# Kernel tuning notes

Measured on AMD Instinct MI355X. Metric: run time of the kernel, lower is better.

Reference implementation:

```python
import jax, jax.numpy as jnp
import numpy as np

HID = 768; HEADS = 12; DH = 64; W = 256  # one-sided window (attention_window=512)
L = 2; VOCAB = 50265; FFN = 3072; NLAB = 8921; B = 2; S = 4096
NEG = -1e9


def _ln(x, s, b):
    m = x.mean(-1, keepdims=True)
    v = ((x - m) ** 2).mean(-1, keepdims=True)
    return (x - m) * jax.lax.rsqrt(v + 1e-5) * s + b


def setup_inputs() -> dict:
    key = jax.random.key(0)
    ks = iter(jax.random.split(key, 64))
    def n(shape, sd=0.02):
        return jax.random.normal(next(ks), shape, jnp.float32) * sd
    inp = {
        'input_ids': jax.random.randint(next(ks), (B, S), 0, VOCAB, dtype=jnp.int32),
        'attention_mask': jnp.ones((B, S), jnp.int32),
        'word_emb': n((VOCAB, HID)), 'pos_emb': n((S, HID)),
        'emb_ln_s': jnp.ones((HID,), jnp.float32), 'emb_ln_b': jnp.zeros((HID,), jnp.float32),
        'Wq': n((L, HID, HID)), 'bq': jnp.zeros((L, HID), jnp.float32),
        'Wk': n((L, HID, HID)), 'bk': jnp.zeros((L, HID), jnp.float32),
        'Wv': n((L, HID, HID)), 'bv': jnp.zeros((L, HID), jnp.float32),
        'Wqg': n((L, HID, HID)), 'bqg': jnp.zeros((L, HID), jnp.float32),
        'Wkg': n((L, HID, HID)), 'bkg': jnp.zeros((L, HID), jnp.float32),
        'Wvg': n((L, HID, HID)), 'bvg': jnp.zeros((L, HID), jnp.float32),
        'Wo': n((L, HID, HID)), 'bo': jnp.zeros((L, HID), jnp.float32),
        'ln1_s': jnp.ones((L, HID), jnp.float32), 'ln1_b': jnp.zeros((L, HID), jnp.float32),
        'W1': n((L, HID, FFN)), 'b1': jnp.zeros((L, FFN), jnp.float32),
        'W2': n((L, FFN, HID)), 'b2': jnp.zeros((L, HID), jnp.float32),
        'ln2_s': jnp.ones((L, HID), jnp.float32), 'ln2_b': jnp.zeros((L, HID), jnp.float32),
        'head_W': n((HID, NLAB)), 'head_b': jnp.zeros((NLAB,), jnp.float32),
    }
    return inp


def _forward(input_ids, attention_mask, word_emb, pos_emb, emb_ln_s, emb_ln_b,
             Wq, bq, Wk, bk, Wv, bv, Wqg, bqg, Wkg, bkg, Wvg, bvg, Wo, bo,
             ln1_s, ln1_b, W1, b1, W2, b2, ln2_s, ln2_b, head_W, head_b):
    Bc, Sc = input_ids.shape
    nc = Sc // W
    scale = 1.0 / np.sqrt(DH).astype(np.float32)
    # embeddings
    x = word_emb[input_ids] + pos_emb[None, :Sc]
    x = _ln(x, emb_ln_s, emb_ln_b)
    # static band masks: query pos c*W+p, key pos (c-1)*W+kk in the 3-chunk layout
    p = jnp.arange(W)
    kk = jnp.arange(3 * W)
    rel = kk[None, :] - W - p[:, None]                     # [W,3W] key_pos - query_pos
    cpos = (jnp.arange(nc)[:, None, None] - 1) * W + kk[None, None, :]  # [nc,1,3W]
    valid = (cpos >= 0) & (cpos < Sc) & (cpos != 0) & (jnp.abs(rel)[None, :, :] <= W)  # [nc,W,3W]
    am_keys = attention_mask[:, jnp.clip(cpos, 0, Sc - 1)] > 0  # [B,nc,1,3W]
    band_mask = valid[None] & am_keys                        # [B,nc,W,3W]

    def split_heads(t):
        return t.reshape(Bc, Sc, HEADS, DH).transpose(0, 2, 1, 3)

    def chunk3(t):  # [B,H,S,D] -> [B,H,nc,3W,D] keys/values of chunks c-1,c,c+1
        tp = jnp.pad(t, ((0, 0), (0, 0), (W, W), (0, 0)))
        tr = tp.reshape(Bc, HEADS, nc + 2, W, DH)
        return jnp.concatenate([tr[:, :, :-2], tr[:, :, 1:-1], tr[:, :, 2:]], axis=3)

    for l in range(L):
        q = split_heads(x @ Wq[l] + bq[l])
        k = split_heads(x @ Wk[l] + bk[l])
        v = split_heads(x @ Wv[l] + bv[l])
        qg = split_heads(x @ Wqg[l] + bqg[l])
        kg = split_heads(x @ Wkg[l] + bkg[l])
        vg = split_heads(x @ Wvg[l] + bvg[l])
        # sliding-window banded scores
        qc = q.reshape(Bc, HEADS, nc, W, DH)
        kc = chunk3(k)
        vc = chunk3(v)
        sc = jnp.einsum('bhcqd,bhckd->bhcqk', qc, kc) * scale   # [B,H,nc,W,3W]
        sc = jnp.where(band_mask[:, None], sc, NEG)
        # extra column: every local query attends to the global (CLS) key
        g_col = jnp.einsum('bhsd,bhd->bhs', q, kg[:, :, 0]) * scale
        full = jnp.concatenate([g_col[..., None], sc.reshape(Bc, HEADS, Sc, 3 * W)], axis=-1)
        probs = jax.nn.softmax(full, axis=-1)
        p_g = probs[..., 0]
        p_b = probs[..., 1:].reshape(Bc, HEADS, nc, W, 3 * W)
        out = jnp.einsum('bhcqk,bhckd->bhcqd', p_b, vc).reshape(Bc, HEADS, Sc, DH)
        out = out + p_g[..., None] * vg[:, :, 0][:, :, None, :]
        # global (CLS) query: full attention over all tokens with global projections
        gs = jnp.einsum('bhd,bhsd->bhs', qg[:, :, 0], kg) * scale
        gs = jnp.where(attention_mask[:, None, :] > 0, gs, NEG)
        gp = jax.nn.softmax(gs, axis=-1)
        out0 = jnp.einsum('bhs,bhsd->bhd', gp, vg)
        out = out.at[:, :, 0, :].set(out0)
        # output proj + residual + LN, then FFN + residual + LN
        attn = out.transpose(0, 2, 1, 3).reshape(Bc, Sc, HID) @ Wo[l] + bo[l]
        x = _ln(x + attn, ln1_s[l], ln1_b[l])
        h = jax.nn.gelu(x @ W1[l] + b1[l], approximate=False) @ W2[l] + b2[l]
        x = _ln(x + h, ln2_s[l], ln2_b[l])
    # head on CLS token (dropout is identity in eval)
    return x[:, 0] @ head_W + head_b


def reference(input_ids, attention_mask, word_emb, pos_emb, emb_ln_s, emb_ln_b,
              Wq, bq, Wk, bk, Wv, bv, Wqg, bqg, Wkg, bkg, Wvg, bvg, Wo, bo,
              ln1_s, ln1_b, W1, b1, W2, b2, ln2_s, ln2_b, head_W, head_b):
    return _forward(input_ids, attention_mask, word_emb, pos_emb, emb_ln_s, emb_ln_b,
                    Wq, bq, Wk, bk, Wv, bv, Wqg, bqg, Wkg, bkg, Wvg, bvg, Wo, bo,
                    ln1_s, ln1_b, W1, b1, W2, b2, ln2_s, ln2_b, head_W, head_b)
```

## Files before the change

### kernel.cpp

```cpp
#include <hip/hip_runtime.h>
#include <hip/hip_bf16.h>
#include <math.h>

#define HIDN 768
#define NHEAD 12
#define DHEAD 64
#define WWIN 256
#define NCHUNK 16
#define NLAYER 2
#define FFND 3072
#define NLABEL 8921
#define NB 2
#define NS 4096
#define NBS (NB*NS)

#define QSTR 3840
#define OQ   0
#define OK_  768
#define OV   1536
#define OKG  2304
#define OVG  3072

typedef __attribute__((ext_vector_type(8))) short bf16x8;
typedef __attribute__((ext_vector_type(4))) float f32x4;

__device__ __forceinline__ float bf2f(unsigned short u){
  union { unsigned int i; float f; } v; v.i = ((unsigned int)u) << 16; return v.f;
}
__device__ __forceinline__ unsigned short f2bf(float f){
  __hip_bfloat16 h = __float2bfloat16(f);
  return *reinterpret_cast<unsigned short*>(&h);
}
__device__ __forceinline__ void unpack2(unsigned int u, float& a, float& b){
  union { unsigned int i; float f; } x, y;
  x.i = u << 16; y.i = u & 0xffff0000u; a = x.f; b = y.f;
}
__device__ __forceinline__ void gld_lds16(const unsigned short* g, unsigned short* l){
  __builtin_amdgcn_global_load_lds((const __attribute__((address_space(1))) unsigned int*)g,
                                   (__attribute__((address_space(3))) unsigned int*)l, 16, 0, 0);
}

__device__ __forceinline__ int xcd_swz(int orig, int nwg){
  int q = nwg >> 3, r = nwg & 7;
  int x = orig & 7, lo = orig >> 3;
  return (x < r ? x*(q+1) : r*(q+1) + (x-r)*q) + lo;
}

#define DPP_ROR_F(x, N) __builtin_bit_cast(float, __builtin_amdgcn_update_dpp( \
    0, __builtin_bit_cast(int, (x)), 0x120 + (N), 0xf, 0xf, true))
__device__ __forceinline__ float rowmax16(float x){
  x = fmaxf(x, DPP_ROR_F(x, 1));
  x = fmaxf(x, DPP_ROR_F(x, 2));
  x = fmaxf(x, DPP_ROR_F(x, 4));
  x = fmaxf(x, DPP_ROR_F(x, 8));
  return x;
}
__device__ __forceinline__ float rowsum16(float x){
  x = x + DPP_ROR_F(x, 1);
  x = x + DPP_ROR_F(x, 2);
  x = x + DPP_ROR_F(x, 4);
  x = x + DPP_ROR_F(x, 8);
  return x;
}

__global__ __launch_bounds__(256) void embed_k(const int* __restrict__ ids,
    const float* __restrict__ we, const float* __restrict__ pe,
    float* __restrict__ y){
  int i = blockIdx.x*256 + threadIdx.x;
  int row = i / HIDN; int d = i - row*HIDN;
  int s = row & (NS-1);
  int id = ids[row];
  y[i] = we[(size_t)id*HIDN + d] + pe[(size_t)s*HIDN + d];
}

__global__ __launch_bounds__(256) void ln_k(const float* A, const float* R,
    const float* __restrict__ sc, const float* __restrict__ bi,
    float* X, unsigned short* XB){
  __shared__ float red[256];
  int row = blockIdx.x, t = threadIdx.x;
  size_t base = (size_t)row*HIDN;
  float v0 = A[base+t], v1 = A[base+t+256], v2 = A[base+t+512];
  if (R){ v0 += R[base+t]; v1 += R[base+t+256]; v2 += R[base+t+512]; }
  red[t] = v0+v1+v2; __syncthreads();
  for (int st=128; st>0; st>>=1){ if (t<st) red[t]+=red[t+st]; __syncthreads(); }
  float mean = red[0] * (1.0f/HIDN); __syncthreads();
  float d0=v0-mean, d1=v1-mean, d2=v2-mean;
  red[t] = d0*d0+d1*d1+d2*d2; __syncthreads();
  for (int st=128; st>0; st>>=1){ if (t<st) red[t]+=red[t+st]; __syncthreads(); }
  float rs = rsqrtf(red[0] * (1.0f/HIDN) + 1e-5f);
  float o0 = d0*rs*sc[t]     + bi[t];
  float o1 = d1*rs*sc[t+256] + bi[t+256];
  float o2 = d2*rs*sc[t+512] + bi[t+512];
  X[base+t]=o0; X[base+t+256]=o1; X[base+t+512]=o2;
  XB[base+t]=f2bf(o0); XB[base+t+256]=f2bf(o1); XB[base+t+512]=f2bf(o2);
}

__global__ __launch_bounds__(256) void transpose_k(const float* __restrict__ src,
    unsigned short* __restrict__ dst, int R, int C){
  __shared__ unsigned short tile[32][33];
  int ct = blockIdx.x*32, rt = blockIdx.y*32;
  int tx = threadIdx.x, ty = threadIdx.y;
  #pragma unroll
  for (int i=0;i<4;i++) tile[ty+i*8][tx] = f2bf(src[(size_t)(rt+ty+i*8)*C + ct + tx]);
  __syncthreads();
  #pragma unroll
  for (int i=0;i<4;i++) dst[(size_t)(ct+ty+i*8)*R + rt + tx] = tile[tx][ty+i*8];
}

__global__ __launch_bounds__(256) void pack_bias_k(const float* __restrict__ bq,
    const float* __restrict__ bk, const float* __restrict__ bv,
    const float* __restrict__ bkg, const float* __restrict__ bvg,
    float* __restrict__ out){
  int i = blockIdx.x*256 + threadIdx.x;
  int l = i / QSTR; int j = i - l*QSTR;
  int seg = j / HIDN, d = j - seg*HIDN;
  const float* src = (seg==0)?bq : (seg==1)?bk : (seg==2)?bv : (seg==3)?bkg : bvg;
  out[i] = src[l*HIDN + d];
}

template<int OUTF32, int GELU>
__global__ __launch_bounds__(256) void gemm128(const unsigned short* __restrict__ A,
    const unsigned short* __restrict__ BT, const float* __restrict__ bias,
    void* __restrict__ Cp, int M, int N, int K){
  __shared__ unsigned short As[128*64];
  __shared__ unsigned short Bs[128*64];
  const int tid = threadIdx.x;
  const int nwg = gridDim.x * gridDim.y;
  const int wg = xcd_swz(blockIdx.y * gridDim.x + blockIdx.x, nwg);
  const int m0 = (wg / gridDim.x) * 128, n0 = (wg % gridDim.x) * 128;
  const int lane = tid & 63, w = tid >> 6;
  const int n = lane & 15, quad = lane >> 4;
  const int wm = (w>>1)*64, wn = (w&1)*64;
  const int lr = lane >> 3, site = lane & 7;
  f32x4 acc[4][4] = {};
  for (int kb=0; kb<K; kb+=64){
    #pragma unroll
    for (int j=0;j<4;j++){
      int rbase = w*32 + j*8;
      int r = rbase + lr;
      int q = site ^ (r & 7);
      gld_lds16(A  + (size_t)(m0+r)*K + kb + q*8, &As[rbase*64]);
      gld_lds16(BT + (size_t)(n0+r)*K + kb + q*8, &Bs[rbase*64]);
    }
    __syncthreads();
    #pragma unroll
    for (int ks=0; ks<2; ks++){
      bf16x8 a[4], b[4];
      #pragma unroll
      for (int i=0;i<4;i++){
        int rm = wm + i*16 + n;
        a[i] = *(const bf16x8*)&As[rm*64 + (((ks*4+quad) ^ (rm&7))<<3)];
        int rn = wn + i*16 + n;
        b[i] = *(const bf16x8*)&Bs[rn*64 + (((ks*4+quad) ^ (rn&7))<<3)];
      }
      #pragma unroll
      for (int mi=0;mi<4;mi++)
      #pragma unroll
      for (int ni=0;ni<4;ni++)
        acc[mi][ni] = __builtin_amdgcn_mfma_f32_16x16x32_bf16(a[mi], b[ni], acc[mi][ni], 0,0,0);
    }
    __syncthreads();
  }
  #pragma unroll
  for (int mi=0; mi<4; mi++)
  #pragma unroll
  for (int ni=0; ni<4; ni++){
    int col = n0 + wn + ni*16 + n;
    float bsv = bias[col];
    #pragma unroll
    for (int rg=0; rg<4; rg++){
      int row = m0 + wm + mi*16 + quad*4 + rg;
      float v = acc[mi][ni][rg] + bsv;
      if (GELU) v = 0.5f*v*(1.0f + erff(v*0.70710678118f));
      if (OUTF32) ((float*)Cp)[(size_t)row*N + col] = v;
      else ((unsigned short*)Cp)[(size_t)row*N + col] = f2bf(v);
    }
  }
}

__global__ __launch_bounds__(256, 2) void band_attn_mfma(
    const unsigned short* __restrict__ qkv, const int* __restrict__ am,
    unsigned short* __restrict__ Out){
  __shared__ unsigned short Kt[64*72];
  __shared__ unsigned short Vt[64*72];
  __shared__ unsigned short Pbuf[4*64*72];
  __shared__ float mk[64];
  __shared__ unsigned short kgs[64];
  __shared__ unsigned short vgs[64];

  const int tid = threadIdx.x;
  const int bid = xcd_swz(blockIdx.x, gridDim.x);
  const int c = bid & (NCHUNK-1);
  const int h = (bid / NCHUNK) % NHEAD;
  const int b = bid / (NCHUNK*NHEAD);
  const int lane = tid & 63, w = tid >> 6;
  const int n = lane & 15, quad = lane >> 4;
  const int qbase = w * 64;
  unsigned short* Pw = Pbuf + w*64*72;

  if (tid < 8)       ((uint4*)kgs)[tid]   = ((const uint4*)(qkv + ((size_t)b*NS)*QSTR + OKG + h*DHEAD))[tid];
  else if (tid < 16) ((uint4*)vgs)[tid-8] = ((const uint4*)(qkv + ((size_t)b*NS)*QSTR + OVG + h*DHEAD))[tid-8];
  __syncthreads();

  bf16x8 aQ[4][2];
  #pragma unroll
  for (int mi=0; mi<4; mi++)
  #pragma unroll
  for (int ks=0; ks<2; ks++)
    aQ[mi][ks] = *(const bf16x8*)(qkv + ((size_t)(b*NS + c*WWIN + qbase + 16*mi + n))*QSTR
                                    + OQ + h*DHEAD + ks*32 + quad*8);

  f32x4 sacc[4] = {};
  #pragma unroll
  for (int ks=0; ks<2; ks++){
    bf16x8 bg = *(const bf16x8*)(kgs + ks*32 + quad*8);
    bf16x8 z8 = {};
    bg = (n == 0) ? bg : z8;
    #pragma unroll
    for (int mi=0; mi<4; mi++)
      sacc[mi] = __builtin_amdgcn_mfma_f32_16x16x32_bf16(aQ[mi][ks], bg, sacc[mi], 0,0,0);
  }
  float mst[4][4], lpt[4][4];
  f32x4 apv[4][4];
  float vgf[4];
  #pragma unroll
  for (int ni=0; ni<4; ni++) vgf[ni] = bf2f(vgs[16*ni + n]);
  #pragma unroll
  for (int mi=0; mi<4; mi++)
  #pragma unroll
  for (int rg=0; rg<4; rg++){
    float sg = __shfl(sacc[mi][rg], lane & 48);
    mst[mi][rg] = sg * 0.125f;
    lpt[mi][rg] = (n == 0) ? 1.0f : 0.0f;
  }
  #pragma unroll
  for (int mi=0; mi<4; mi++)
  #pragma unroll
  for (int ni=0; ni<4; ni++)
  #pragma unroll
  for (int rg=0; rg<4; rg++) apv[mi][ni][rg] = vgf[ni];

  for (int t=0; t<12; t++){
    __syncthreads();
    {
      int i = tid >> 2, d0 = (tid & 3) * 8;
      int kp = (c-1)*WWIN + t*64 + i;
      int kpc = min(max(kp, 0), NS-1);
      size_t gb = ((size_t)(b*NS + kpc))*QSTR + h*DHEAD;
      uint4 k0 = *(const uint4*)(qkv + gb + OK_ + d0);
      uint4 k1 = *(const uint4*)(qkv + gb + OK_ + d0 + 32);
      uint4 v0 = *(const uint4*)(qkv + gb + OV + d0);
      uint4 v1 = *(const uint4*)(qkv + gb + OV + d0 + 32);
      *(uint4*)(Kt + i*72 + d0) = k0;
      *(uint4*)(Kt + i*72 + d0 + 32) = k1;
      const unsigned short* s0 = (const unsigned short*)&v0;
      const unsigned short* s1 = (const unsigned short*)&v1;
      #pragma unroll
      for (int j=0;j<8;j++){
        Vt[(d0+j)*72 + i] = s0[j];
        Vt[(d0+32+j)*72 + i] = s1[j];
      }
      if ((tid & 3) == 0)
        mk[i] = (kp >= 1 && kp < NS && am[b*NS + kpc] > 0) ? 0.0f : -1e9f;
    }
    __syncthreads();

    float mkv[4];
    #pragma unroll
    for (int ni=0; ni<4; ni++) mkv[ni] = mk[16*ni + n];

    f32x4 accs[4][4] = {};
    #pragma unroll
    for (int ks=0; ks<2; ks++){
      bf16x8 bK[4];
      #pragma unroll
      for (int ni=0; ni<4; ni++)
        bK[ni] = *(const bf16x8*)(Kt + (16*ni + n)*72 + ks*32 + quad*8);
      #pragma unroll
      for (int mi=0; mi<4; mi++)
      #pragma unroll
      for (int ni=0; ni<4; ni++)
        accs[mi][ni] = __builtin_amdgcn_mfma_f32_16x16x32_bf16(aQ[mi][ks], bK[ni], accs[mi][ni], 0,0,0);
    }

    #pragma unroll
    for (int mi=0; mi<4; mi++){
      float sv[4][4];
      #pragma unroll
      for (int ni=0; ni<4; ni++)
      #pragma unroll
      for (int rg=0; rg<4; rg++){
        int kk = t*64 + 16*ni + n;
        int pr = qbase + 16*mi + quad*4 + rg;
        float s = accs[mi][ni][rg]*0.125f + mkv[ni];
        if ((unsigned)(kk - pr) > 512u) s = -1e9f;
        sv[ni][rg] = s;
      }
      #pragma unroll
      for (int rg=0; rg<4; rg++){
        float rm = fmaxf(fmaxf(sv[0][rg], sv[1][rg]), fmaxf(sv[2][rg], sv[3][rg]));
        rm = rowmax16(rm);
        float mold = mst[mi][rg];
        float mnew = fmaxf(mold, rm);
        float alpha = __expf(mold - mnew);
        mst[mi][rg] = mnew;
        float psum = 0.f;
        #pragma unroll
        for (int ni=0; ni<4; ni++){
          float pv = __expf(sv[ni][rg] - mnew);
          sv[ni][rg] = pv;
          psum += pv;
        }
        lpt[mi][rg] = lpt[mi][rg]*alpha + psum;
        #pragma unroll
        for (int ni=0; ni<4; ni++) apv[mi][ni][rg] *= alpha;
        int prow = 16*mi + quad*4 + rg;
        #pragma unroll
        for (int ni=0; ni<4; ni++)
          Pw[prow*72 + 16*ni + n] = f2bf(sv[ni][rg]);
      }
    }

    #pragma unroll
    for (int ks2=0; ks2<2; ks2++){
      bf16x8 aP[4], bV[4];
      #pragma unroll
      for (int mi=0; mi<4; mi++)
        aP[mi] = *(const bf16x8*)(Pw + (16*mi + n)*72 + ks2*32 + quad*8);
      #pragma unroll
      for (int ni=0; ni<4; ni++)
        bV[ni] = *(const bf16x8*)(Vt + (16*ni + n)*72 + ks2*32 + quad*8);
      #pragma unroll
      for (int mi=0; mi<4; mi++)
      #pragma unroll
      for (int ni=0; ni<4; ni++)
        apv[mi][ni] = __builtin_amdgcn_mfma_f32_16x16x32_bf16(aP[mi], bV[ni], apv[mi][ni], 0,0,0);
    }
  }

  #pragma unroll
  for (int mi=0; mi<4; mi++)
  #pragma unroll
  for (int rg=0; rg<4; rg++){
    float L = rowsum16(lpt[mi][rg]);
    float inv = 1.0f / L;
    int q = c*WWIN + qbase + 16*mi + quad*4 + rg;
    size_t ob = ((size_t)(b*NS + q))*HIDN + h*DHEAD;
    #pragma unroll
    for (int ni=0; ni<4; ni++)
      Out[ob + 16*ni + n] = f2bf(apv[mi][ni][rg] * inv);
  }
}

__global__ __launch_bounds__(128) void gattn_part(
    const unsigned short* __restrict__ QG0, const unsigned short* __restrict__ qkv,
    const int* __restrict__ am, float* __restrict__ part){
  __shared__ float qs[64];
  __shared__ float ps[128];
  __shared__ float red[128];
  int t = threadIdx.x;
  int cx = blockIdx.x, h = blockIdx.y, b = blockIdx.z;
  if (t < 32){
    float a, bb; unpack2(((const unsigned int*)(QG0 + (size_t)b*128*HIDN + h*DHEAD))[t], a, bb);
    qs[2*t]=a*0.125f; qs[2*t+1]=bb*0.125f;
  }
  __syncthreads();
  int kp = cx*128 + t;
  const unsigned int* kr = (const unsigned int*)(qkv + ((size_t)(b*NS+kp))*QSTR + OKG + h*DHEAD);
  float sv = 0.f;
  #pragma unroll
  for (int j=0;j<32;j++){ float a,bb; unpack2(kr[j],a,bb); sv += qs[2*j]*a + qs[2*j+1]*bb; }
  if (am[b*NS+kp] <= 0) sv = -1e9f;
  red[t] = sv; __syncthreads();
  for (int st=64; st>0; st>>=1){ if (t<st) red[t] = fmaxf(red[t], red[t+st]); __syncthreads(); }
  float M = red[0]; __syncthreads();
  float e = __expf(sv - M);
  ps[t] = e; red[t] = e; __syncthreads();
  for (int st=64; st>0; st>>=1){ if (t<st) red[t] += red[t+st]; __syncthreads(); }
  float L = red[0];
  float* po = part + ((size_t)((b*NHEAD+h)*32 + cx))*66;
  if (t==0){ po[0]=M; po[1]=L; }
  if (t < 64){
    float o = 0.f;
    #pragma unroll 4
    for (int i=0;i<128;i++)
      o += ps[i] * bf2f(qkv[((size_t)(b*NS + cx*128 + i))*QSTR + OVG + h*DHEAD + t]);
    po[2+t] = o;
  }
}

__global__ __launch_bounds__(64) void gattn_reduce(const float* __restrict__ part,
    unsigned short* __restrict__ Out){
  int bh = blockIdx.x;
  int b = bh / NHEAD, h = bh % NHEAD;
  int d = threadIdx.x;
  const float* pp = part + (size_t)bh*32*66;
  float M = -1e30f;
  for (int c2=0;c2<32;c2++) M = fmaxf(M, pp[c2*66]);
  float L = 0.f, o = 0.f;
  for (int c2=0;c2<32;c2++){
    float w = __expf(pp[c2*66] - M);
    L += pp[c2*66+1]*w;
    o += pp[c2*66+2+d]*w;
  }
  Out[((size_t)b*NS)*HIDN + h*DHEAD + d] = f2bf(o / L);
}

__global__ __launch_bounds__(256) void head_k(const float* __restrict__ X,
    const float* __restrict__ HW, const float* __restrict__ HB,
    float* __restrict__ Outp){
  int n = blockIdx.x*256 + threadIdx.x;
  int b = blockIdx.y;
  if (n >= NLABEL) return;
  const float* x0 = X + (size_t)b*NS*HIDN;
  float a = HB[n];
  #pragma unroll 8
  for (int d=0; d<HIDN; d++) a += x0[d] * HW[(size_t)d*NLABEL + n];
  Outp[(size_t)b*NLABEL + n] = a;
}

extern "C" void kernel_launch(void* const* d_in, const int* in_sizes, int n_in,
                              void* d_out, int out_size, void* d_ws, size_t ws_size,
                              hipStream_t stream){
  (void)in_sizes; (void)n_in; (void)out_size; (void)ws_size;
  const int* ids = (const int*)d_in[0];
  const int* am  = (const int*)d_in[1];
  const float* we  = (const float*)d_in[2];
  const float* pe  = (const float*)d_in[3];
  const float* elns= (const float*)d_in[4];
  const float* elnb= (const float*)d_in[5];
  const float* Wq  = (const float*)d_in[6];
  const float* bq  = (const float*)d_in[7];
  const float* Wk  = (const float*)d_in[8];
  const float* bk  = (const float*)d_in[9];
  const float* Wv  = (const float*)d_in[10];
  const float* bv  = (const float*)d_in[11];
  const float* Wqg = (const float*)d_in[12];
  const float* bqg = (const float*)d_in[13];
  const float* Wkg = (const float*)d_in[14];
  const float* bkg = (const float*)d_in[15];
  const float* Wvg = (const float*)d_in[16];
  const float* bvg = (const float*)d_in[17];
  const float* Wo  = (const float*)d_in[18];
  const float* bo  = (const float*)d_in[19];
  const float* l1s = (const float*)d_in[20];
  const float* l1b = (const float*)d_in[21];
  const float* W1  = (const float*)d_in[22];
  const float* b1  = (const float*)d_in[23];
  const float* W2  = (const float*)d_in[24];
  const float* b2  = (const float*)d_in[25];
  const float* l2s = (const float*)d_in[26];
  const float* l2b = (const float*)d_in[27];
  const float* hW  = (const float*)d_in[28];
  const float* hB  = (const float*)d_in[29];

  char* ws = (char*)d_ws;
  float* x = (float*)ws;
  float* y = (float*)(ws + 25165824);
  unsigned short* xb   = (unsigned short*)(ws + 50331648);
  unsigned short* qkvb = (unsigned short*)(ws + 62914560);
  unsigned short* qg0b = (unsigned short*)(ws + 125829120);
  float* part = (float*)(ws + 126222336);
  unsigned short* ao   = (unsigned short*)(ws + 126425088);
  unsigned short* hbuf = (unsigned short*)(ws + 139008000);
  unsigned short* wt   = (unsigned short*)(ws + 189339648);
  float* bpack = (float*)(ws + 224729088);

  const size_t SQ = 589824;
  const size_t SW = 2359296;
  const size_t PERL = 7*SQ + 2*SW;

  auto tr = [&](const float* src, unsigned short* dst, int R, int C){
    dim3 g(C/32, R/32), blk(32, 8);
    transpose_k<<<g, blk, 0, stream>>>(src, dst, R, C);
  };
  for (int l=0; l<NLAYER; l++){
    unsigned short* base = wt + (size_t)l*PERL;
    tr(Wq  + (size_t)l*SQ, base + 0*SQ, 768, 768);
    tr(Wk  + (size_t)l*SQ, base + 1*SQ, 768, 768);
    tr(Wv  + (size_t)l*SQ, base + 2*SQ, 768, 768);
    tr(Wkg + (size_t)l*SQ, base + 3*SQ, 768, 768);
    tr(Wvg + (size_t)l*SQ, base + 4*SQ, 768, 768);
    tr(Wqg + (size_t)l*SQ, base + 5*SQ, 768, 768);
    tr(Wo  + (size_t)l*SQ, base + 6*SQ, 768, 768);
    tr(W1  + (size_t)l*SW, base + 7*SQ, 768, 3072);
    tr(W2  + (size_t)l*SW, base + 7*SQ + SW, 3072, 768);
  }
  pack_bias_k<<<(NLAYER*QSTR)/256, 256, 0, stream>>>(bq, bk, bv, bkg, bvg, bpack);

  embed_k<<<(NBS*HIDN)/256, 256, 0, stream>>>(ids, we, pe, y);
  ln_k<<<NBS, 256, 0, stream>>>(y, nullptr, elns, elnb, x, xb);

  for (int l=0; l<NLAYER; l++){
    unsigned short* base = wt + (size_t)l*PERL;
    gemm128<0,0><<<dim3(30,64), 256, 0, stream>>>(xb, base, bpack + (size_t)l*QSTR,
                                                  qkvb, NBS, QSTR, 768);
    for (int b=0; b<NB; b++)
      gemm128<0,0><<<dim3(6,1), 256, 0, stream>>>(xb + (size_t)b*NS*HIDN, base + 5*SQ,
                                                  bqg + l*768, qg0b + (size_t)b*128*HIDN,
                                                  128, 768, 768);
    band_attn_mfma<<<NB*NHEAD*NCHUNK, 256, 0, stream>>>(qkvb, am, ao);
    gattn_part<<<dim3(32, NHEAD, NB), 128, 0, stream>>>(qg0b, qkvb, am, part);
    gattn_reduce<<<NB*NHEAD, 64, 0, stream>>>(part, ao);
    gemm128<1,0><<<dim3(6,64), 256, 0, stream>>>(ao, base + 6*SQ, bo + l*768, y, NBS, 768, 768);
    ln_k<<<NBS, 256, 0, stream>>>(y, x, l1s + l*768, l1b + l*768, x, xb);
    gemm128<0,1><<<dim3(24,64), 256, 0, stream>>>(xb, base + 7*SQ, b1 + l*3072, hbuf, NBS, 3072, 768);
    gemm128<1,0><<<dim3(6,64), 256, 0, stream>>>(hbuf, base + 7*SQ + SW, b2 + l*768, y, NBS, 768, 3072);
    ln_k<<<NBS, 256, 0, stream>>>(y, x, l2s + l*768, l2b + l*768, x, xb);
  }

  head_k<<<dim3((NLABEL+255)/256, NB), 256, 0, stream>>>(x, hW, hB, (float*)d_out);
}
```

Measured before the change: 1.173 ms.

## Add 256x256 double-buffered GEMM for QKV and FFN1, split-K head

Adds a 512-thread GEMM kernel with 256x256 output tiles and double-buffered LDS staging, used for the wide QKV projection and the FFN up-projection. The larger tiles raise data reuse per block and overlap the next tile's loads with the current MFMA work. The classifier head kernel is also rewritten to cache the CLS vector in shared memory and split the 768-long reduction across four thread groups, giving more blocks and parallelism. In exchange, the new GEMM uses 128KB of LDS per block and launches far fewer blocks, which may reduce occupancy and load balance on the device.

```diff
diff --git a/kernel.cpp b/kernel.cpp
--- a/kernel.cpp
+++ b/kernel.cpp
@@ -169,6 +169,81 @@
     float bsv = bias[col];
     #pragma unroll
     for (int rg=0; rg<4; rg++){
+      int row = m0 + wm + mi*16 + quad*4 + rg;
+      float v = acc[mi][ni][rg] + bsv;
+      if (GELU) v = 0.5f*v*(1.0f + erff(v*0.70710678118f));
+      if (OUTF32) ((float*)Cp)[(size_t)row*N + col] = v;
+      else ((unsigned short*)Cp)[(size_t)row*N + col] = f2bf(v);
+    }
+  }
+}
+
+template<int OUTF32, int GELU>
+__global__ __launch_bounds__(512) void gemm256(const unsigned short* __restrict__ A,
+    const unsigned short* __restrict__ BT, const float* __restrict__ bias,
+    void* __restrict__ Cp, int M, int N, int K){
+  __shared__ unsigned short AsB[2][256*64];
+  __shared__ unsigned short BsB[2][256*64];
+  const int tid = threadIdx.x;
+  const int gx = gridDim.x;
+  const int nwg = gx * gridDim.y;
+  const int wg = xcd_swz(blockIdx.y*gx + blockIdx.x, nwg);
+  const int m0 = (wg / gx) * 256, n0 = (wg % gx) * 256;
+  const int lane = tid & 63, w = tid >> 6;
+  const int n = lane & 15, quad = lane >> 4;
+  const int wm = (w>>2)*128, wn = (w&3)*64;
+  const int lr = lane >> 3, site = lane & 7;
+  const int NK = K >> 6;
+  f32x4 acc[8][4] = {};
+
+  auto stage = [&](int b, int kb){
+    #pragma unroll
+    for (int j=0;j<4;j++){
+      int rbase = w*32 + j*8;
+      int r = rbase + lr;
+      int q = site ^ (r & 7);
+      gld_lds16(A  + (size_t)(m0+r)*K + kb + q*8, &AsB[b][rbase*64]);
+      gld_lds16(BT + (size_t)(n0+r)*K + kb + q*8, &BsB[b][rbase*64]);
+    }
+  };
+
+  stage(0, 0);
+  __syncthreads();
+  for (int kt=0; kt<NK; ++kt){
+    const int b = kt & 1;
+    if (kt+1 < NK) stage(b^1, (kt+1)<<6);
+    const unsigned short* As_ = AsB[b];
+    const unsigned short* Bs_ = BsB[b];
+    bf16x8 bfr[2][4];
+    #pragma unroll
+    for (int ks=0;ks<2;ks++)
+    #pragma unroll
+    for (int ni=0;ni<4;ni++){
+      int rn = wn + ni*16 + n;
+      bfr[ks][ni] = *(const bf16x8*)&Bs_[rn*64 + (((ks*4+quad) ^ (rn&7))<<3)];
+    }
+    #pragma unroll
+    for (int mi=0;mi<8;mi++){
+      int rm = wm + mi*16 + n;
+      bf16x8 a0 = *(const bf16x8*)&As_[rm*64 + (((quad)     ^ (rm&7))<<3)];
+      bf16x8 a1 = *(const bf16x8*)&As_[rm*64 + (((4+quad)   ^ (rm&7))<<3)];
+      #pragma unroll
+      for (int ni=0;ni<4;ni++)
+        acc[mi][ni] = __builtin_amdgcn_mfma_f32_16x16x32_bf16(a0, bfr[0][ni], acc[mi][ni],0,0,0);
+      #pragma unroll
+      for (int ni=0;ni<4;ni++)
+        acc[mi][ni] = __builtin_amdgcn_mfma_f32_16x16x32_bf16(a1, bfr[1][ni], acc[mi][ni],0,0,0);
+    }
+    if (kt+1 < NK) __syncthreads();
+  }
+  #pragma unroll
+  for (int mi=0;mi<8;mi++)
+  #pragma unroll
+  for (int ni=0;ni<4;ni++){
+    int col = n0 + wn + ni*16 + n;
+    float bsv = bias[col];
+    #pragma unroll
+    for (int rg=0;rg<4;rg++){
       int row = m0 + wm + mi*16 + quad*4 + rg;
       float v = acc[mi][ni][rg] + bsv;
       if (GELU) v = 0.5f*v*(1.0f + erff(v*0.70710678118f));
@@ -409,14 +484,25 @@
 __global__ __launch_bounds__(256) void head_k(const float* __restrict__ X,
     const float* __restrict__ HW, const float* __restrict__ HB,
     float* __restrict__ Outp){
-  int n = blockIdx.x*256 + threadIdx.x;
+  __shared__ float red[256];
+  __shared__ float xs[HIDN];
   int b = blockIdx.y;
-  if (n >= NLABEL) return;
+  int base = blockIdx.x*64;
+  int t = threadIdx.x;
   const float* x0 = X + (size_t)b*NS*HIDN;
-  float a = HB[n];
-  #pragma unroll 8
-  for (int d=0; d<HIDN; d++) a += x0[d] * HW[(size_t)d*NLABEL + n];
-  Outp[(size_t)b*NLABEL + n] = a;
+  for (int i=t; i<HIDN; i+=256) xs[i] = x0[i];
+  __syncthreads();
+  int n = base + (t & 63);
+  int dp = t >> 6;
+  float a = 0.f;
+  if (n < NLABEL){
+    #pragma unroll 4
+    for (int d=dp*192; d<dp*192+192; ++d)
+      a += xs[d] * HW[(size_t)d*NLABEL + n];
+  }
+  red[t] = a; __syncthreads();
+  if (t < 64 && n < NLABEL)
+    Outp[(size_t)b*NLABEL + n] = red[t]+red[t+64]+red[t+128]+red[t+192] + HB[n];
 }
 
 extern "C" void kernel_launch(void* const* d_in, const int* in_sizes, int n_in,
@@ -493,7 +579,7 @@
 
   for (int l=0; l<NLAYER; l++){
     unsigned short* base = wt + (size_t)l*PERL;
-    gemm128<0,0><<<dim3(30,64), 256, 0, stream>>>(xb, base, bpack + (size_t)l*QSTR,
+    gemm256<0,0><<<dim3(15,32), 512, 0, stream>>>(xb, base, bpack + (size_t)l*QSTR,
                                                   qkvb, NBS, QSTR, 768);
     for (int b=0; b<NB; b++)
       gemm128<0,0><<<dim3(6,1), 256, 0, stream>>>(xb + (size_t)b*NS*HIDN, base + 5*SQ,
@@ -504,10 +590,10 @@
     gattn_reduce<<<NB*NHEAD, 64, 0, stream>>>(part, ao);
     gemm128<1,0><<<dim3(6,64), 256, 0, stream>>>(ao, base + 6*SQ, bo + l*768, y, NBS, 768, 768);
     ln_k<<<NBS, 256, 0, stream>>>(y, x, l1s + l*768, l1b + l*768, x, xb);
-    gemm128<0,1><<<dim3(24,64), 256, 0, stream>>>(xb, base + 7*SQ, b1 + l*3072, hbuf, NBS, 3072, 768);
+    gemm256<0,1><<<dim3(12,32), 512, 0, stream>>>(xb, base + 7*SQ, b1 + l*3072, hbuf, NBS, 3072, 768);
     gemm128<1,0><<<dim3(6,64), 256, 0, stream>>>(hbuf, base + 7*SQ + SW, b2 + l*768, y, NBS, 768, 3072);
     ln_k<<<NBS, 256, 0, stream>>>(y, x, l2s + l*768, l2b + l*768, x, xb);
   }
 
-  head_k<<<dim3((NLABEL+255)/256, NB), 256, 0, stream>>>(x, hW, hB, (float*)d_out);
-}
+  head_k<<<dim3((NLABEL+63)/64, NB), 256, 0, stream>>>(x, hW, hB, (float*)d_out);
+}
```

After: 1.301 ms. 11.0% more time.
